# Performance work log

Measured on AMD Instinct MI355X. Metric: run time of the kernel, lower is better.

## Reference

```python
import jax, jax.numpy as jnp
import numpy as np

B, H, L, T = 256, 1024, 2, 128


def _spectral_normalize(W, u):
    # torch spectral_norm with n_power_iterations=1: u, v are detached buffers;
    # sigma = u' W v, weight used is W / sigma. W: [4H, H], u: [4H].
    v = W.T @ u
    v = v / (jnp.linalg.norm(v) + 1e-12)
    u2 = W @ v
    u2 = u2 / (jnp.linalg.norm(u2) + 1e-12)
    u2 = jax.lax.stop_gradient(u2)
    v = jax.lax.stop_gradient(v)
    sigma = u2 @ (W @ v)
    return W / sigma


def setup_inputs() -> dict:
    key = jax.random.key(0)
    ks = jax.random.split(key, 9)
    bound = 1.0 / np.sqrt(H)  # torch LSTM default init: U(-1/sqrt(H), 1/sqrt(H))
    inp = {
        "initial_input": jax.random.normal(ks[0], (B, 1, H), jnp.float32),
        "h0": jax.random.normal(ks[1], (L, B, H), jnp.float32),
        "c0": jax.random.normal(ks[2], (L, B, H), jnp.float32),
        "W_ih": jax.random.uniform(ks[3], (L, 4 * H, H), jnp.float32, -bound, bound),
        "W_hh": jax.random.uniform(ks[4], (L, 4 * H, H), jnp.float32, -bound, bound),
        "b_ih": jax.random.uniform(ks[5], (L, 4 * H), jnp.float32, -bound, bound),
        "b_hh": jax.random.uniform(ks[6], (L, 4 * H), jnp.float32, -bound, bound),
        "u_ih": jax.random.normal(ks[7], (L, 4 * H), jnp.float32),
        "u_hh": jax.random.normal(ks[8], (L, 4 * H), jnp.float32),
        "length": T,
    }
    inp["u_ih"] = inp["u_ih"] / jnp.linalg.norm(inp["u_ih"], axis=-1, keepdims=True)
    inp["u_hh"] = inp["u_hh"] / jnp.linalg.norm(inp["u_hh"], axis=-1, keepdims=True)
    return inp


def reference(initial_input, h0, c0, W_ih, W_hh, b_ih, b_hh, u_ih, u_hh, length):
    n_layers = W_ih.shape[0]
    # Spectrally-normalized weights (computed once, reused every step).
    Wih = jax.vmap(_spectral_normalize)(W_ih, u_ih)  # [L, 4H, H]
    Whh = jax.vmap(_spectral_normalize)(W_hh, u_hh)  # [L, 4H, H]
    bias = b_ih + b_hh  # [L, 4H]

    def cell(x, h, c, l):
        # torch gate order: i, f, g, o
        gates = x @ Wih[l].T + h @ Whh[l].T + bias[l]  # [B, 4H]
        i, f, g, o = jnp.split(gates, 4, axis=-1)
        c_new = jax.nn.sigmoid(f) * c + jax.nn.sigmoid(i) * jnp.tanh(g)
        h_new = jax.nn.sigmoid(o) * jnp.tanh(c_new)
        return h_new, c_new

    def step(carry, _):
        x, h, c = carry  # x: [B,H]; h, c: [L,B,H]
        hs, cs = [], []
        inp = x
        for l in range(n_layers):
            h_new, c_new = cell(inp, h[l], c[l], l)
            hs.append(h_new)
            cs.append(c_new)
            inp = h_new  # top-layer output feeds back as next-step input
        return (inp, jnp.stack(hs), jnp.stack(cs)), inp

    x0 = initial_input[:, 0, :]  # seq dim is 1
    _, ys = jax.lax.scan(step, (x0, h0, c0), None, length=length)
    return jnp.transpose(ys, (1, 0, 2))  # [B, length, H]
```

## Files before the change

### kernel.cpp

```cpp
#include <hip/hip_runtime.h>
#include <hip/hip_bf16.h>


typedef _Float16 half8 __attribute__((ext_vector_type(8)));
typedef _Float16 half4 __attribute__((ext_vector_type(4)));
typedef float f32x4 __attribute__((ext_vector_type(4)));

#define HSZ 1024
#define BSZ 256
#define TSZ 128

#define AS1 __attribute__((address_space(1)))
#define AS3 __attribute__((address_space(3)))

static __device__ __forceinline__ void gload16(const void* g, void* l) {
  __builtin_amdgcn_global_load_lds((const AS1 unsigned int*)g,
                                   (AS3 unsigned int*)l, 16, 0, 0);
}

__global__ __launch_bounds__(256) void prep_vraw1(
    const float* __restrict__ Wih, const float* __restrict__ Whh,
    const float* __restrict__ uih, const float* __restrict__ uhh,
    float* __restrict__ vpart) {
  int bx = blockIdx.x;
  int m = bx >> 6, rc = (bx >> 2) & 15, jc = bx & 3;
  int j = jc * 256 + threadIdx.x;
  const float* W = (m < 2 ? Wih : Whh) + ((size_t)(m & 1) << 22);
  const float* u = (m < 2 ? uih : uhh) + (m & 1) * 4096;
  float acc = 0.f;
  int rbase = rc * 256;
  for (int r = 0; r < 256; ++r)
    acc += W[(size_t)(rbase + r) * 1024 + j] * u[rbase + r];
  vpart[(m * 16 + rc) * 1024 + j] = acc;
}

__global__ __launch_bounds__(256) void prep_vraw2(
    const float* __restrict__ vpart, float* __restrict__ vraw) {
  int i = blockIdx.x * 256 + threadIdx.x;
  int m = i >> 10;
  float acc = 0.f;
  for (int rc = 0; rc < 16; ++rc)
    acc += vpart[(m * 16 + rc) * 1024 + (i & 1023)];
  vraw[i] = acc;
}

__global__ __launch_bounds__(256) void prep_wv(
    const float* __restrict__ Wih, const float* __restrict__ Whh,
    const float* __restrict__ vraw, float* __restrict__ wv) {
  int m = blockIdx.y;
  int w = threadIdx.x >> 6, l = threadIdx.x & 63;
  int r = blockIdx.x * 4 + w;
  const float* W = (m < 2 ? Wih : Whh) + ((size_t)(m & 1) << 22) + (size_t)r * 1024;
  const float* v = vraw + m * 1024;
  float acc = 0.f;
  for (int it = 0; it < 4; ++it) {
    int j = it * 256 + l * 4;
    float4 w4 = *(const float4*)(W + j);
    float4 v4 = *(const float4*)(v + j);
    acc += w4.x * v4.x + w4.y * v4.y + w4.z * v4.z + w4.w * v4.w;
  }
  for (int o = 32; o; o >>= 1) acc += __shfl_down(acc, o);
  if (l == 0) wv[m * 4096 + r] = acc;
}

__global__ __launch_bounds__(256) void prep_sig(
    const float* __restrict__ vraw, const float* __restrict__ wv,
    float* __restrict__ invsig) {
  int m = blockIdx.x, tid = threadIdx.x;
  __shared__ float red[256];
  float sv = 0.f, sw = 0.f;
  for (int i = tid; i < 1024; i += 256) { float x = vraw[m * 1024 + i]; sv += x * x; }
  for (int i = tid; i < 4096; i += 256) { float x = wv[m * 4096 + i]; sw += x * x; }
  red[tid] = sv; __syncthreads();
  for (int s = 128; s; s >>= 1) { if (tid < s) red[tid] += red[tid + s]; __syncthreads(); }
  float svt = red[0]; __syncthreads();
  red[tid] = sw; __syncthreads();
  for (int s = 128; s; s >>= 1) { if (tid < s) red[tid] += red[tid + s]; __syncthreads(); }
  if (tid == 0) invsig[m] = sqrtf(svt / red[0]);
}

__global__ __launch_bounds__(256) void prep_wcomb(
    const float* __restrict__ Wih, const float* __restrict__ Whh,
    const float* __restrict__ invsig, _Float16* __restrict__ wcomb) {
  size_t idx4 = ((size_t)blockIdx.x * 256 + threadIdx.x) * 4;
  if (idx4 >= (size_t)2 * 4096 * 2048) return;
  int l = (int)(idx4 >> 23);
  int rem = (int)(idx4 & ((1u << 23) - 1));
  int r = rem >> 11, k = rem & 2047;
  const float* src; float s;
  if (k < 1024) { src = Wih + ((size_t)l << 22) + (size_t)r * 1024 + k; s = invsig[l]; }
  else          { src = Whh + ((size_t)l << 22) + (size_t)r * 1024 + (k - 1024); s = invsig[2 + l]; }
  float4 v = *(const float4*)src;
  half4 o = { (_Float16)(v.x * s), (_Float16)(v.y * s),
              (_Float16)(v.z * s), (_Float16)(v.w * s) };
  *(half4*)(wcomb + idx4) = o;
}

__global__ __launch_bounds__(256) void prep_bias(
    const float* __restrict__ b_ih, const float* __restrict__ b_hh,
    float* __restrict__ bias) {
  int i = blockIdx.x * 256 + threadIdx.x;
  if (i < 8192) bias[i] = b_ih[i] + b_hh[i];
}

__global__ __launch_bounds__(256) void prep_init(
    const float* __restrict__ x0, const float* __restrict__ h0,
    const float* __restrict__ c0, _Float16* __restrict__ Xinit,
    _Float16* __restrict__ H0p0, _Float16* __restrict__ H1p0,
    float* __restrict__ C0, float* __restrict__ C1) {
  int i = blockIdx.x * 256 + threadIdx.x;
  Xinit[i] = (_Float16)x0[i];
  H0p0[i]  = (_Float16)h0[i];
  H1p0[i]  = (_Float16)h0[262144 + i];
  C0[i] = c0[i];
  C1[i] = c0[262144 + i];
}

__global__ __launch_bounds__(256) void lstm_cell(
    const _Float16* __restrict__ W,
    const float* __restrict__ bias,
    const _Float16* __restrict__ xbuf,
    const _Float16* __restrict__ hbuf,
    float* __restrict__ cbuf,
    _Float16* __restrict__ hout,
    float* __restrict__ yout)
{
  __shared__ __align__(16) char smem[98304];
  const int tid = threadIdx.x;
  const int lane = tid & 63, w = tid >> 6;
  const int wr = w & 1, wc = w >> 1;
  const int lr = lane & 15, lk = lane >> 4;
  const int j0 = blockIdx.x * 16;
  const int bm0 = blockIdx.y * 64;

  const char* Wb = (const char*)W;
  const char* Xb = (const char*)xbuf;
  const char* Hc = (const char*)hbuf;

  size_t abase[4];
  int    brow[4];
  int    bswz[4];
  int    dst16[4];
#pragma unroll
  for (int q = 0; q < 4; ++q) {
    int c = q * 256 + tid;
    int row = c >> 4, g16 = c & 15;
    int srcg = (g16 ^ (row & 7)) << 4;
    int grow = (row >> 4) * 1024 + j0 + (row & 15);
    abase[q] = (size_t)grow * 4096 + srcg;
    brow[q] = row; bswz[q] = srcg;
    dst16[q] = c * 16;
  }

  f32x4 acc00 = {0,0,0,0}, acc01 = {0,0,0,0}, acc10 = {0,0,0,0}, acc11 = {0,0,0,0};
  const int ar0 = wr * 32 + lr, ar1 = ar0 + 16;
  const int br0 = wc * 32 + lr, br1 = br0 + 16;

#define STAGE(p, bi) do {                                                     \
    const char* actb = ((bi) < 8) ? Xb : Hc;                                  \
    const size_t k0b = (size_t)((bi) & 7) * 256;                              \
    const size_t ka  = (size_t)(bi) * 256;                                    \
    char* lb = smem + (p) * 32768;                                            \
    _Pragma("unroll")                                                         \
    for (int q = 0; q < 4; ++q) {                                             \
      gload16(Wb + abase[q] + ka, lb + dst16[q]);                             \
      gload16(actb + (size_t)(bm0 + brow[q]) * 2048 + k0b + bswz[q],          \
              lb + 16384 + dst16[q]);                                         \
    }                                                                         \
  } while (0)

#define LDSOFF(row, s) ((row) * 256 + (((((s) << 2) + lk) ^ ((row) & 7)) << 4))

#define COMPUTE(p) do {                                                       \
    const _Float16* Ab = (const _Float16*)(smem + (p) * 32768);               \
    const _Float16* Bb = (const _Float16*)(smem + (p) * 32768 + 16384);       \
    _Pragma("unroll")                                                         \
    for (int s = 0; s < 4; ++s) {                                             \
      half8 a0 = *(const half8*)(Ab + (LDSOFF(ar0, s) >> 1));                 \
      half8 a1 = *(const half8*)(Ab + (LDSOFF(ar1, s) >> 1));                 \
      half8 b0 = *(const half8*)(Bb + (LDSOFF(br0, s) >> 1));                 \
      half8 b1 = *(const half8*)(Bb + (LDSOFF(br1, s) >> 1));                 \
      acc00 = __builtin_amdgcn_mfma_f32_16x16x32_f16(a0, b0, acc00, 0, 0, 0); \
      acc01 = __builtin_amdgcn_mfma_f32_16x16x32_f16(a0, b1, acc01, 0, 0, 0); \
      acc10 = __builtin_amdgcn_mfma_f32_16x16x32_f16(a1, b0, acc10, 0, 0, 0); \
      acc11 = __builtin_amdgcn_mfma_f32_16x16x32_f16(a1, b1, acc11, 0, 0, 0); \
    }                                                                         \
  } while (0)

#define WAITVM(N) asm volatile("s_waitcnt vmcnt(" #N ")" ::: "memory")
#define BAR() do { asm volatile("" ::: "memory");                             \
    __builtin_amdgcn_s_barrier();                                             \
    asm volatile("" ::: "memory"); } while (0)

  STAGE(0, 0);
  STAGE(1, 1);

#define ITER(bi, pb, ps) do {                                                 \
    STAGE(ps, (bi) + 2);                                                      \
    WAITVM(16); BAR();                                                        \
    COMPUTE(pb);                                                              \
    BAR(); } while (0)

  ITER(0, 0, 2);  ITER(1, 1, 0);  ITER(2, 2, 1);  ITER(3, 0, 2);
  ITER(4, 1, 0);  ITER(5, 2, 1);  ITER(6, 0, 2);  ITER(7, 1, 0);
  ITER(8, 2, 1);  ITER(9, 0, 2);  ITER(10, 1, 0); ITER(11, 2, 1);
  ITER(12, 0, 2); ITER(13, 1, 0);
  WAITVM(8);  BAR(); COMPUTE(2); BAR();
  WAITVM(0);  BAR(); COMPUTE(0); BAR();

  float (*gl)[65] = (float(*)[65])smem;
#pragma unroll
  for (int i = 0; i < 2; ++i) {
    const int rbase = wr * 32 + i * 16 + lk * 4;
    f32x4 v0 = (i == 0) ? acc00 : acc10;
    f32x4 v1 = (i == 0) ? acc01 : acc11;
#pragma unroll
    for (int rr = 0; rr < 4; ++rr) {
      gl[rbase + rr][wc * 32 + lr] = v0[rr];
      gl[rbase + rr][wc * 32 + 16 + lr] = v1[rr];
    }
  }
  __syncthreads();

  {
    const int b = tid >> 2, jj = tid & 3;
    const float* bp = bias + j0 + jj * 4;
    float4 bi4 = *(const float4*)(bp);
    float4 bf4 = *(const float4*)(bp + 1024);
    float4 bg4 = *(const float4*)(bp + 2048);
    float4 bo4 = *(const float4*)(bp + 3072);
    const size_t idx = (size_t)(bm0 + b) * 1024 + j0 + jj * 4;
    float4 c4 = *(const float4*)&cbuf[idx];
    float cn4[4], hn4[4];
    const float* bi_p = &bi4.x; const float* bf_p = &bf4.x;
    const float* bg_p = &bg4.x; const float* bo_p = &bo4.x;
    const float* c_p = &c4.x;
#pragma unroll
    for (int cc = 0; cc < 4; ++cc) {
      const int r = jj * 4 + cc;
      float iv = gl[r][b]      + bi_p[cc];
      float fv = gl[16 + r][b] + bf_p[cc];
      float gv = gl[32 + r][b] + bg_p[cc];
      float ov = gl[48 + r][b] + bo_p[cc];
      float si = 1.f / (1.f + __expf(-iv));
      float sf = 1.f / (1.f + __expf(-fv));
      float so = 1.f / (1.f + __expf(-ov));
      float e2g = __expf(fminf(fmaxf(2.f * gv, -30.f), 30.f));
      float tg = (e2g - 1.f) / (e2g + 1.f);
      float cn = sf * c_p[cc] + si * tg;
      float e2c = __expf(fminf(fmaxf(2.f * cn, -30.f), 30.f));
      float tc = (e2c - 1.f) / (e2c + 1.f);
      cn4[cc] = cn;
      hn4[cc] = so * tc;
    }
    float4 cno = { cn4[0], cn4[1], cn4[2], cn4[3] };
    *(float4*)&cbuf[idx] = cno;
    half4 h4 = { (_Float16)hn4[0], (_Float16)hn4[1],
                 (_Float16)hn4[2], (_Float16)hn4[3] };
    *(half4*)&hout[idx] = h4;
    if (yout) {
      float4 y4 = { hn4[0], hn4[1], hn4[2], hn4[3] };
      *(float4*)&yout[(size_t)(bm0 + b) * (TSZ * HSZ) + j0 + jj * 4] = y4;
    }
  }
#undef STAGE
#undef LDSOFF
#undef COMPUTE
#undef WAITVM
#undef BAR
#undef ITER
}

extern "C" void kernel_launch(void* const* d_in, const int* in_sizes, int n_in,
                              void* d_out, int out_size, void* d_ws, size_t ws_size,
                              hipStream_t stream) {
  (void)in_sizes; (void)n_in; (void)out_size; (void)ws_size;
  const float* x0   = (const float*)d_in[0];
  const float* h0   = (const float*)d_in[1];
  const float* c0   = (const float*)d_in[2];
  const float* Wih  = (const float*)d_in[3];
  const float* Whh  = (const float*)d_in[4];
  const float* b_ih = (const float*)d_in[5];
  const float* b_hh = (const float*)d_in[6];
  const float* u_ih = (const float*)d_in[7];
  const float* u_hh = (const float*)d_in[8];
  float* out = (float*)d_out;

  char* ws = (char*)d_ws;
  size_t off = 0;
  auto alloc = [&](size_t bytes) -> void* {
    void* p = ws + off;
    off = (off + bytes + 255) & ~(size_t)255;
    return p;
  };
  _Float16* wcomb  = (_Float16*)alloc((size_t)2 * 4096 * 2048 * 2);
  float*    vpart  = (float*)alloc((size_t)4 * 16 * 1024 * 4);
  float*    vraw   = (float*)alloc((size_t)4 * 1024 * 4);
  float*    wv     = (float*)alloc((size_t)4 * 4096 * 4);
  float*    invsig = (float*)alloc(16);
  float*    bias   = (float*)alloc((size_t)2 * 4096 * 4);
  _Float16* Xinit  = (_Float16*)alloc((size_t)262144 * 2);
  _Float16* Hb[2][2];
  for (int a = 0; a < 2; ++a)
    for (int p = 0; p < 2; ++p)
      Hb[a][p] = (_Float16*)alloc((size_t)262144 * 2);
  float* Cb[2];
  Cb[0] = (float*)alloc((size_t)262144 * 4);
  Cb[1] = (float*)alloc((size_t)262144 * 4);

  prep_vraw1<<<256, 256, 0, stream>>>(Wih, Whh, u_ih, u_hh, vpart);
  prep_vraw2<<<16, 256, 0, stream>>>(vpart, vraw);
  prep_wv<<<dim3(1024, 4), 256, 0, stream>>>(Wih, Whh, vraw, wv);
  prep_sig<<<4, 256, 0, stream>>>(vraw, wv, invsig);
  prep_wcomb<<<16384, 256, 0, stream>>>(Wih, Whh, invsig, wcomb);
  prep_bias<<<32, 256, 0, stream>>>(b_ih, b_hh, bias);
  prep_init<<<1024, 256, 0, stream>>>(x0, h0, c0, Xinit, Hb[0][0], Hb[1][0], Cb[0], Cb[1]);

  _Float16* W0 = wcomb;
  _Float16* W1 = wcomb + (size_t)4096 * 2048;

  for (int t = 0; t < TSZ; ++t) {
    int p = t & 1;
    lstm_cell<<<dim3(64, 4), 256, 0, stream>>>(
        W0, bias, (t == 0 ? Xinit : Hb[1][p]), Hb[0][p], Cb[0], Hb[0][p ^ 1], nullptr);
    lstm_cell<<<dim3(64, 4), 256, 0, stream>>>(
        W1, bias + 4096, Hb[0][p ^ 1], Hb[1][p], Cb[1], Hb[1][p ^ 1],
        out + (size_t)t * HSZ);
  }
}
```

Before: 2.723 ms.

## Fuse all timestep launches into one persistent kernel with per-group atomic barriers

Replaces the 256 per-step lstm_cell launches with a single persistent kernel of 256 blocks. Each block loops over all timesteps and layers. Blocks covering the same 64-row batch slice synchronise through a per-phase atomic counter barrier, since each batch group only depends on its own rows. This removes kernel launch gaps and lets different batch groups drift apart in time. In exchange it relies on all 256 blocks being co-resident, or the spin barrier will deadlock, and it adds spin and sleep overhead at every phase.

Measured after the change: 5.743 ms. +110.9%, slower.

```diff
diff --git a/kernel.cpp b/kernel.cpp
--- a/kernel.cpp
+++ b/kernel.cpp
@@ -9,6 +9,8 @@
 #define HSZ 1024
 #define BSZ 256
 #define TSZ 128
+#define NBLK 256
+#define GRP 64
 
 #define AS1 __attribute__((address_space(1)))
 #define AS3 __attribute__((address_space(3)))
@@ -116,41 +118,24 @@
   C1[i] = c0[262144 + i];
 }
 
-__global__ __launch_bounds__(256) void lstm_cell(
-    const _Float16* __restrict__ W,
-    const float* __restrict__ bias,
-    const _Float16* __restrict__ xbuf,
-    const _Float16* __restrict__ hbuf,
-    float* __restrict__ cbuf,
-    _Float16* __restrict__ hout,
-    float* __restrict__ yout)
-{
-  __shared__ __align__(16) char smem[98304];
-  const int tid = threadIdx.x;
-  const int lane = tid & 63, w = tid >> 6;
-  const int wr = w & 1, wc = w >> 1;
-  const int lr = lane & 15, lk = lane >> 4;
-  const int j0 = blockIdx.x * 16;
-  const int bm0 = blockIdx.y * 64;
-
-  const char* Wb = (const char*)W;
-  const char* Xb = (const char*)xbuf;
-  const char* Hc = (const char*)hbuf;
-
+struct Desc {
   size_t abase[4];
   int    brow[4];
   int    bswz[4];
   int    dst16[4];
-#pragma unroll
-  for (int q = 0; q < 4; ++q) {
-    int c = q * 256 + tid;
-    int row = c >> 4, g16 = c & 15;
-    int srcg = (g16 ^ (row & 7)) << 4;
-    int grow = (row >> 4) * 1024 + j0 + (row & 15);
-    abase[q] = (size_t)grow * 4096 + srcg;
-    brow[q] = row; bswz[q] = srcg;
-    dst16[q] = c * 16;
-  }
+};
+
+static __device__ __forceinline__ void cell_phase(
+    const _Float16* __restrict__ W, const float* __restrict__ bs,
+    const _Float16* __restrict__ xbuf, const _Float16* __restrict__ hbuf,
+    float* __restrict__ cbuf, _Float16* __restrict__ hout, float* yout,
+    char* smem, const Desc& d, int j0, int bm0, int tid) {
+  const int lane = tid & 63, w = tid >> 6;
+  const int wr = w & 1, wc = w >> 1;
+  const int lr = lane & 15, lk = lane >> 4;
+  const char* Wb = (const char*)W;
+  const char* Xb = (const char*)xbuf;
+  const char* Hc = (const char*)hbuf;
 
   f32x4 acc00 = {0,0,0,0}, acc01 = {0,0,0,0}, acc10 = {0,0,0,0}, acc11 = {0,0,0,0};
   const int ar0 = wr * 32 + lr, ar1 = ar0 + 16;
@@ -163,9 +148,9 @@
     char* lb = smem + (p) * 32768;                                            \
     _Pragma("unroll")                                                         \
     for (int q = 0; q < 4; ++q) {                                             \
-      gload16(Wb + abase[q] + ka, lb + dst16[q]);                             \
-      gload16(actb + (size_t)(bm0 + brow[q]) * 2048 + k0b + bswz[q],          \
-              lb + 16384 + dst16[q]);                                         \
+      gload16(Wb + d.abase[q] + ka, lb + d.dst16[q]);                         \
+      gload16(actb + (size_t)(bm0 + d.brow[q]) * 2048 + k0b + d.bswz[q],      \
+              lb + 16384 + d.dst16[q]);                                       \
     }                                                                         \
   } while (0)
 
@@ -224,7 +209,7 @@
 
   {
     const int b = tid >> 2, jj = tid & 3;
-    const float* bp = bias + j0 + jj * 4;
+    const float* bp = bs + j0 + jj * 4;
     float4 bi4 = *(const float4*)(bp);
     float4 bf4 = *(const float4*)(bp + 1024);
     float4 bg4 = *(const float4*)(bp + 2048);
@@ -271,6 +256,62 @@
 #undef ITER
 }
 
+static __device__ __forceinline__ void group_barrier(unsigned* flag) {
+  __syncthreads();
+  if (threadIdx.x == 0) {
+    __hip_atomic_fetch_add(flag, 1u, __ATOMIC_RELEASE, __HIP_MEMORY_SCOPE_AGENT);
+    while (__hip_atomic_load(flag, __ATOMIC_RELAXED, __HIP_MEMORY_SCOPE_AGENT) < GRP)
+      __builtin_amdgcn_s_sleep(2);
+    (void)__hip_atomic_load(flag, __ATOMIC_ACQUIRE, __HIP_MEMORY_SCOPE_AGENT);
+  }
+  __syncthreads();
+}
+
+__global__ __launch_bounds__(256) void lstm_persist(
+    const _Float16* __restrict__ W0, const _Float16* __restrict__ W1,
+    const float* __restrict__ bias, const _Float16* __restrict__ Xinit,
+    _Float16* __restrict__ H00, _Float16* __restrict__ H01,
+    _Float16* __restrict__ H10, _Float16* __restrict__ H11,
+    float* __restrict__ C0, float* __restrict__ C1,
+    float* __restrict__ out, unsigned* __restrict__ flags) {
+  __shared__ __align__(16) char smem[98304];
+  const int tid = threadIdx.x;
+  const int bx = blockIdx.x;
+  const int j0 = (bx & 63) * 16;
+  const int bm0 = (bx >> 6) * 64;
+  const int grp = bx >> 6;
+
+  Desc d;
+#pragma unroll
+  for (int q = 0; q < 4; ++q) {
+    int c = q * 256 + tid;
+    int row = c >> 4, g16 = c & 15;
+    int srcg = (g16 ^ (row & 7)) << 4;
+    int grow = (row >> 4) * 1024 + j0 + (row & 15);
+    d.abase[q] = (size_t)grow * 4096 + srcg;
+    d.brow[q] = row; d.bswz[q] = srcg;
+    d.dst16[q] = c * 16;
+  }
+
+  _Float16* H0[2] = { H00, H01 };
+  _Float16* H1[2] = { H10, H11 };
+
+#pragma unroll 1
+  for (int ph = 0; ph < 2 * TSZ; ++ph) {
+    const int t = ph >> 1, layer = ph & 1, p = t & 1;
+    if (layer == 0) {
+      cell_phase(W0, bias,
+                 (t == 0 ? Xinit : H1[p]), H0[p], C0, H0[p ^ 1], nullptr,
+                 smem, d, j0, bm0, tid);
+    } else {
+      cell_phase(W1, bias + 4096,
+                 H0[p ^ 1], H1[p], C1, H1[p ^ 1], out + (size_t)t * HSZ,
+                 smem, d, j0, bm0, tid);
+    }
+    if (ph != 2 * TSZ - 1) group_barrier(flags + (ph * 4 + grp) * 16);
+  }
+}
+
 extern "C" void kernel_launch(void* const* d_in, const int* in_sizes, int n_in,
                               void* d_out, int out_size, void* d_ws, size_t ws_size,
                               hipStream_t stream) {
@@ -307,6 +348,7 @@
   float* Cb[2];
   Cb[0] = (float*)alloc((size_t)262144 * 4);
   Cb[1] = (float*)alloc((size_t)262144 * 4);
+  unsigned* flags = (unsigned*)alloc(2 * TSZ * 4 * 16 * sizeof(unsigned));
 
   prep_vraw1<<<256, 256, 0, stream>>>(Wih, Whh, u_ih, u_hh, vpart);
   prep_vraw2<<<16, 256, 0, stream>>>(vpart, vraw);
@@ -315,16 +357,12 @@
   prep_wcomb<<<16384, 256, 0, stream>>>(Wih, Whh, invsig, wcomb);
   prep_bias<<<32, 256, 0, stream>>>(b_ih, b_hh, bias);
   prep_init<<<1024, 256, 0, stream>>>(x0, h0, c0, Xinit, Hb[0][0], Hb[1][0], Cb[0], Cb[1]);
+  hipMemsetAsync(flags, 0, 2 * TSZ * 4 * 16 * sizeof(unsigned), stream);
 
   _Float16* W0 = wcomb;
   _Float16* W1 = wcomb + (size_t)4096 * 2048;
 
-  for (int t = 0; t < TSZ; ++t) {
-    int p = t & 1;
-    lstm_cell<<<dim3(64, 4), 256, 0, stream>>>(
-        W0, bias, (t == 0 ? Xinit : Hb[1][p]), Hb[0][p], Cb[0], Hb[0][p ^ 1], nullptr);
-    lstm_cell<<<dim3(64, 4), 256, 0, stream>>>(
-        W1, bias + 4096, Hb[0][p ^ 1], Hb[1][p], Cb[1], Hb[1][p ^ 1],
-        out + (size_t)t * HSZ);
-  }
-}
+  lstm_persist<<<dim3(NBLK), dim3(256), 0, stream>>>(
+      W0, W1, bias, Xinit, Hb[0][0], Hb[0][1], Hb[1][0], Hb[1][1],
+      Cb[0], Cb[1], out, flags);
+}
```
